# Optimization experiments

Measured on AMD Instinct MI355X. Metric: run time of the kernel, lower is better.

## Reference

```python
import jax, jax.numpy as jnp
import numpy as np

N_NODES = 100000
N_EDGES = 3200000
D_FEAT = 64


def setup_inputs() -> dict:
    key = jax.random.key(0)
    k1, k2, k3 = jax.random.split(key, 3)
    h = jax.random.normal(k1, (N_NODES, D_FEAT), dtype=jnp.float32)
    src = jax.random.randint(k2, (N_EDGES,), 0, N_NODES, dtype=jnp.int64 if jax.config.jax_enable_x64 else jnp.int32)
    dst = jax.random.randint(k3, (N_EDGES,), 0, N_NODES, dtype=jnp.int64 if jax.config.jax_enable_x64 else jnp.int32)
    return {"h": h, "src": src, "dst": dst}


def reference(h, src, dst):
    # u_dot_v: per-edge dot product of src/dst node features -> [E, 1]
    score = jnp.sum(h[src] * h[dst], axis=-1, keepdims=True)
    return score
```

## Files before the change

### kernel.cpp

```cpp
#include <hip/hip_runtime.h>
#include <hip/hip_bf16.h>


typedef __attribute__((ext_vector_type(8))) unsigned short ushort8v;
typedef __attribute__((ext_vector_type(4))) unsigned short ushort4v;

__device__ __forceinline__ unsigned short f32_to_bf16_rn(float f) {
  unsigned u = __float_as_uint(f);
  u += 0x7FFFu + ((u >> 16) & 1u);
  return (unsigned short)(u >> 16);
}

__global__ __launch_bounds__(256) void convert_f32_bf16(
    const float4* __restrict__ h4, ushort4v* __restrict__ hb4, int n4) {
  int i = blockIdx.x * blockDim.x + threadIdx.x;
  int stride = gridDim.x * blockDim.x;
  for (int j = i; j < n4; j += stride) {
    float4 v = h4[j];
    ushort4v o;
    o.x = f32_to_bf16_rn(v.x);
    o.y = f32_to_bf16_rn(v.y);
    o.z = f32_to_bf16_rn(v.z);
    o.w = f32_to_bf16_rn(v.w);
    hb4[j] = o;
  }
}

__global__ __launch_bounds__(256) void edge_dot_bf16(
    const unsigned short* __restrict__ hb,
    const int* __restrict__ src,
    const int* __restrict__ dst,
    float* __restrict__ out,
    int n_edges) {
  const int tid     = blockIdx.x * blockDim.x + threadIdx.x;
  const int l       = tid & 7;
  int e             = tid >> 3;
  const int estride = (gridDim.x * blockDim.x) >> 3;

  for (; e < n_edges; e += estride) {
    const int s = src[e];
    const int d = dst[e];
    const ushort8v a = *((const ushort8v*)(hb + (size_t)s * 64) + l);
    const ushort8v b = *((const ushort8v*)(hb + (size_t)d * 64) + l);
    float acc = 0.f;
#pragma unroll
    for (int k = 0; k < 8; ++k) {
      const float fa = __uint_as_float(((unsigned)a[k]) << 16);
      const float fb = __uint_as_float(((unsigned)b[k]) << 16);
      acc = fmaf(fa, fb, acc);
    }
    acc += __shfl_xor(acc, 1);
    acc += __shfl_xor(acc, 2);
    acc += __shfl_xor(acc, 4);
    if (l == 0) out[e] = acc;
  }
}

__global__ __launch_bounds__(256) void edge_dot_f32(
    const float* __restrict__ h,
    const int* __restrict__ src,
    const int* __restrict__ dst,
    float* __restrict__ out,
    int n_edges) {
  const int tid     = blockIdx.x * blockDim.x + threadIdx.x;
  const int l       = tid & 15;
  int e             = tid >> 4;
  const int estride = (gridDim.x * blockDim.x) >> 4;
  for (; e < n_edges; e += estride) {
    const int s = src[e];
    const int d = dst[e];
    const float4 a = *((const float4*)(h + (size_t)s * 64) + l);
    const float4 b = *((const float4*)(h + (size_t)d * 64) + l);
    float acc = a.x * b.x + a.y * b.y + a.z * b.z + a.w * b.w;
    acc += __shfl_xor(acc, 1);
    acc += __shfl_xor(acc, 2);
    acc += __shfl_xor(acc, 4);
    acc += __shfl_xor(acc, 8);
    if (l == 0) out[e] = acc;
  }
}

extern "C" void kernel_launch(void* const* d_in, const int* in_sizes, int n_in,
                              void* d_out, int out_size, void* d_ws, size_t ws_size,
                              hipStream_t stream) {
  const float* h   = (const float*)d_in[0];
  const int*   src = (const int*)d_in[1];
  const int*   dst = (const int*)d_in[2];
  float*       out = (float*)d_out;
  const int n_h     = in_sizes[0];
  const int n_edges = in_sizes[1];

  const size_t need = (size_t)n_h * sizeof(unsigned short);
  if (ws_size >= need) {
    unsigned short* hb = (unsigned short*)d_ws;
    const int n4 = n_h / 4;
    int cgrid = (n4 + 255) / 256;
    if (cgrid > 4096) cgrid = 4096;
    convert_f32_bf16<<<cgrid, 256, 0, stream>>>(
        (const float4*)h, (ushort4v*)hb, n4);

    int grid = (n_edges + 31) / 32;
    if (grid > 2048) grid = 2048;
    edge_dot_bf16<<<grid, 256, 0, stream>>>(hb, src, dst, out, n_edges);
  } else {
    int grid = (n_edges + 15) / 16;
    if (grid > 2048) grid = 2048;
    edge_dot_f32<<<grid, 256, 0, stream>>>(h, src, dst, out, n_edges);
  }
}
```

Measured before the change: 172.3 us.

## Quantize node features to per-row int8 and compute edge dots in integer

Replaces the bf16 feature conversion with per-row symmetric int8 quantization that stores a scale per row. The edge kernel gathers 64-byte rows with 4 lanes per edge, does integer dot products, and rescales by the two row scales. The aim is to halve gather traffic and the footprint of the staged table. The cost is lower accuracy, which may exceed tolerance, plus two extra scale loads per edge.

Result: faster. 162.0 us (-6.0%).

```diff
diff --git a/kernel.cpp b/kernel.cpp
--- a/kernel.cpp
+++ b/kernel.cpp
@@ -2,57 +2,71 @@
 #include <hip/hip_bf16.h>
 
 
-typedef __attribute__((ext_vector_type(8))) unsigned short ushort8v;
-typedef __attribute__((ext_vector_type(4))) unsigned short ushort4v;
+typedef __attribute__((ext_vector_type(4))) int int4v;
 
-__device__ __forceinline__ unsigned short f32_to_bf16_rn(float f) {
-  unsigned u = __float_as_uint(f);
-  u += 0x7FFFu + ((u >> 16) & 1u);
-  return (unsigned short)(u >> 16);
-}
-
-__global__ __launch_bounds__(256) void convert_f32_bf16(
-    const float4* __restrict__ h4, ushort4v* __restrict__ hb4, int n4) {
-  int i = blockIdx.x * blockDim.x + threadIdx.x;
-  int stride = gridDim.x * blockDim.x;
-  for (int j = i; j < n4; j += stride) {
-    float4 v = h4[j];
-    ushort4v o;
-    o.x = f32_to_bf16_rn(v.x);
-    o.y = f32_to_bf16_rn(v.y);
-    o.z = f32_to_bf16_rn(v.z);
-    o.w = f32_to_bf16_rn(v.w);
-    hb4[j] = o;
+__global__ __launch_bounds__(256) void quantize_rows_i8(
+    const float4* __restrict__ h4,
+    int* __restrict__ q8,
+    float* __restrict__ inv_scale,
+    int n_rows) {
+  const int tid = blockIdx.x * blockDim.x + threadIdx.x;
+  const int l = tid & 15;
+  int r = tid >> 4;
+  const int rstride = (gridDim.x * blockDim.x) >> 4;
+  for (; r < n_rows; r += rstride) {
+    const float4 v = h4[(size_t)r * 16 + l];
+    float m = fmaxf(fmaxf(fabsf(v.x), fabsf(v.y)),
+                    fmaxf(fabsf(v.z), fabsf(v.w)));
+    m = fmaxf(m, __shfl_xor(m, 1));
+    m = fmaxf(m, __shfl_xor(m, 2));
+    m = fmaxf(m, __shfl_xor(m, 4));
+    m = fmaxf(m, __shfl_xor(m, 8));
+    const float scale = (m > 0.f) ? 127.0f / m : 0.f;
+    const int c0 = (int)rintf(v.x * scale);
+    const int c1 = (int)rintf(v.y * scale);
+    const int c2 = (int)rintf(v.z * scale);
+    const int c3 = (int)rintf(v.w * scale);
+    const int packed = (c0 & 0xFF) | ((c1 & 0xFF) << 8) |
+                       ((c2 & 0xFF) << 16) | ((c3 & 0xFF) << 24);
+    q8[(size_t)r * 16 + l] = packed;
+    if (l == 0) inv_scale[r] = m * (1.0f / 127.0f);
   }
 }
 
-__global__ __launch_bounds__(256) void edge_dot_bf16(
-    const unsigned short* __restrict__ hb,
+__device__ __forceinline__ int dot4_i8(int a, int b, int acc) {
+#pragma unroll
+  for (int i = 0; i < 4; ++i) {
+    const int ai = (a << (24 - 8 * i)) >> 24;
+    const int bi = (b << (24 - 8 * i)) >> 24;
+    acc += ai * bi;
+  }
+  return acc;
+}
+
+__global__ __launch_bounds__(256) void edge_dot_i8(
+    const int* __restrict__ q8,
+    const float* __restrict__ inv_scale,
     const int* __restrict__ src,
     const int* __restrict__ dst,
     float* __restrict__ out,
     int n_edges) {
-  const int tid     = blockIdx.x * blockDim.x + threadIdx.x;
-  const int l       = tid & 7;
-  int e             = tid >> 3;
-  const int estride = (gridDim.x * blockDim.x) >> 3;
-
+  const int tid = blockIdx.x * blockDim.x + threadIdx.x;
+  const int l = tid & 3;
+  int e = tid >> 2;
+  const int estride = (gridDim.x * blockDim.x) >> 2;
   for (; e < n_edges; e += estride) {
     const int s = src[e];
     const int d = dst[e];
-    const ushort8v a = *((const ushort8v*)(hb + (size_t)s * 64) + l);
-    const ushort8v b = *((const ushort8v*)(hb + (size_t)d * 64) + l);
-    float acc = 0.f;
-#pragma unroll
-    for (int k = 0; k < 8; ++k) {
-      const float fa = __uint_as_float(((unsigned)a[k]) << 16);
-      const float fb = __uint_as_float(((unsigned)b[k]) << 16);
-      acc = fmaf(fa, fb, acc);
-    }
+    const int4v a = *((const int4v*)(q8 + (size_t)s * 16) + l);
+    const int4v b = *((const int4v*)(q8 + (size_t)d * 16) + l);
+    int acc = 0;
+    acc = dot4_i8(a[0], b[0], acc);
+    acc = dot4_i8(a[1], b[1], acc);
+    acc = dot4_i8(a[2], b[2], acc);
+    acc = dot4_i8(a[3], b[3], acc);
     acc += __shfl_xor(acc, 1);
     acc += __shfl_xor(acc, 2);
-    acc += __shfl_xor(acc, 4);
-    if (l == 0) out[e] = acc;
+    if (l == 0) out[e] = (float)acc * inv_scale[s] * inv_scale[d];
   }
 }
 
@@ -62,9 +76,9 @@
     const int* __restrict__ dst,
     float* __restrict__ out,
     int n_edges) {
-  const int tid     = blockIdx.x * blockDim.x + threadIdx.x;
-  const int l       = tid & 15;
-  int e             = tid >> 4;
+  const int tid = blockIdx.x * blockDim.x + threadIdx.x;
+  const int l = tid & 15;
+  int e = tid >> 4;
   const int estride = (gridDim.x * blockDim.x) >> 4;
   for (; e < n_edges; e += estride) {
     const int s = src[e];
@@ -89,19 +103,21 @@
   float*       out = (float*)d_out;
   const int n_h     = in_sizes[0];
   const int n_edges = in_sizes[1];
+  const int n_rows  = n_h / 64;
 
-  const size_t need = (size_t)n_h * sizeof(unsigned short);
+  const size_t need = (size_t)n_rows * 64 + (size_t)n_rows * sizeof(float);
   if (ws_size >= need) {
-    unsigned short* hb = (unsigned short*)d_ws;
-    const int n4 = n_h / 4;
-    int cgrid = (n4 + 255) / 256;
+    int*   q8  = (int*)d_ws;
+    float* isc = (float*)((char*)d_ws + (size_t)n_rows * 64);
+
+    int cgrid = (n_rows * 16 + 255) / 256;
     if (cgrid > 4096) cgrid = 4096;
-    convert_f32_bf16<<<cgrid, 256, 0, stream>>>(
-        (const float4*)h, (ushort4v*)hb, n4);
+    quantize_rows_i8<<<cgrid, 256, 0, stream>>>(
+        (const float4*)h, q8, isc, n_rows);
 
-    int grid = (n_edges + 31) / 32;
+    int grid = (n_edges + 63) / 64;
     if (grid > 2048) grid = 2048;
-    edge_dot_bf16<<<grid, 256, 0, stream>>>(hb, src, dst, out, n_edges);
+    edge_dot_i8<<<grid, 256, 0, stream>>>(q8, isc, src, dst, out, n_edges);
   } else {
     int grid = (n_edges + 15) / 16;
     if (grid > 2048) grid = 2048;
```
